# Kernel optimization log

Measured on AMD Instinct MI355X. Metric: run time of the kernel, lower is better.

The kernel has to match this reference:

```python
import jax, jax.numpy as jnp
import numpy as np

BLOCKSIZE = 4096
OUT_FEATURES = 16384
IN_FEATURES = 4096
BATCH, SEQ = 4, 2048


def setup_inputs() -> dict:
    key = jax.random.key(0)
    k_x, k_w, k_a, k_b = jax.random.split(key, 4)
    x = jax.random.normal(k_x, (BATCH, SEQ, IN_FEATURES), dtype=jnp.float32)
    # quantized int8 weight stored as indices into the 256-entry codebook
    weight_q = jax.random.randint(k_w, (OUT_FEATURES, IN_FEATURES), 0, 256, dtype=jnp.int32)
    n_blocks = (OUT_FEATURES * IN_FEATURES) // BLOCKSIZE  # 16384
    absmax = jax.random.uniform(k_a, (n_blocks,), dtype=jnp.float32) + 0.5
    # bitsandbytes dynamic-map code: a sorted table of values in [-1, 1]
    code = jnp.linspace(-1.0, 1.0, 256, dtype=jnp.float32)
    bias = jax.random.normal(k_b, (OUT_FEATURES,), dtype=jnp.float32) * 0.02
    return {"x": x, "weight_q": weight_q, "absmax": absmax, "code": code, "bias": bias}


def dequantize_blockwise(weight_q, absmax, code):
    # codebook lookup then per-block absmax scaling
    flat = code[weight_q.reshape(-1)]                      # [out*in]
    flat = flat.reshape(-1, BLOCKSIZE) * absmax[:, None]   # [n_blocks, blocksize]
    return flat.reshape(weight_q.shape)                    # [out, in]


def reference(x, weight_q, absmax, code, bias):
    w = dequantize_blockwise(weight_q, absmax, code)       # [out, in] fp32
    # F.linear(x, w, bias) = x @ w.T + bias
    return jnp.einsum("bsi,oi->bso", x, w) + bias
```

## Files before the change

kernel.cpp:

```cpp
#include <hip/hip_runtime.h>
#include <hip/hip_bf16.h>
#include <stdint.h>

#define M_TOTAL 8192
#define N_TOTAL 16384
#define K_TOTAL 4096

#define BM 256
#define BN 256
#define BK 64
#define NKT (K_TOTAL / BK)

using f32x4  = __attribute__((ext_vector_type(4))) float;
using bf16x8 = __attribute__((ext_vector_type(8))) short;

#define UNROLL _Pragma("unroll")

__device__ __forceinline__ unsigned short f2bf(float f) {
    union { float f; unsigned u; } v; v.f = f;
    unsigned r = v.u + 0x7fffu + ((v.u >> 16) & 1u);
    return (unsigned short)(r >> 16);
}

__device__ __forceinline__ void gload_lds16(const void* g, void* l) {
    __builtin_amdgcn_global_load_lds(
        (const __attribute__((address_space(1))) unsigned int*)g,
        (__attribute__((address_space(3))) unsigned int*)l,
        16, 0, 0);
}

__global__ void dequant_w_kernel(const int* __restrict__ q,
                                 const float* __restrict__ am,
                                 const float* __restrict__ code,
                                 unsigned short* __restrict__ wb) {
    __shared__ float lc[256];
    if (threadIdx.x < 256) lc[threadIdx.x] = code[threadIdx.x];
    __syncthreads();
    const int total = (N_TOTAL / 4) * K_TOTAL;
    const int stride = gridDim.x * blockDim.x;
    for (int i = blockIdx.x * blockDim.x + threadIdx.x; i < total; i += stride) {
        int4 v = reinterpret_cast<const int4*>(q)[i];
        float a = am[i >> 10];
        ushort4 o;
        o.x = f2bf(lc[v.x & 255] * a);
        o.y = f2bf(lc[v.y & 255] * a);
        o.z = f2bf(lc[v.z & 255] * a);
        o.w = f2bf(lc[v.w & 255] * a);
        reinterpret_cast<ushort4*>(wb)[i] = o;
    }
}

__global__ void cvt_x_kernel(const float* __restrict__ x,
                             unsigned short* __restrict__ xb) {
    const int total = (M_TOTAL * K_TOTAL) / 4;
    const int stride = gridDim.x * blockDim.x;
    for (int i = blockIdx.x * blockDim.x + threadIdx.x; i < total; i += stride) {
        float4 v = reinterpret_cast<const float4*>(x)[i];
        ushort4 o;
        o.x = f2bf(v.x); o.y = f2bf(v.y); o.z = f2bf(v.z); o.w = f2bf(v.w);
        reinterpret_cast<ushort4*>(xb)[i] = o;
    }
}

#define LOAD_A(DST, BUFI, MH)                                                     \
    UNROLL for (int mf = 0; mf < 4; ++mf)                                         \
        UNROLL for (int ks = 0; ks < 2; ++ks)                                     \
            DST[mf][ks] = *reinterpret_cast<const bf16x8*>(                       \
                &sA[BUFI][((MH)*128 + arow_base + mf*16)*BK +                     \
                          (((ks*4 + rslot_hi) ^ rslot_xor)*8)]);

#define LOAD_B(DST, BUFI, NH)                                                     \
    UNROLL for (int nf = 0; nf < 2; ++nf)                                         \
        UNROLL for (int ks = 0; ks < 2; ++ks)                                     \
            DST[nf][ks] = *reinterpret_cast<const bf16x8*>(                       \
                &sB[BUFI][((NH)*128 + brow_base + nf*16)*BK +                     \
                          (((ks*4 + rslot_hi) ^ rslot_xor)*8)]);

#define MFMA_Q(MH, NH, AR, BR)                                                    \
    UNROLL for (int mf = 0; mf < 4; ++mf)                                         \
        UNROLL for (int nf = 0; nf < 2; ++nf) {                                   \
            acc[MH][mf][NH][nf] = __builtin_amdgcn_mfma_f32_16x16x32_bf16(        \
                AR[mf][0], BR[nf][0], acc[MH][mf][NH][nf], 0, 0, 0);              \
            acc[MH][mf][NH][nf] = __builtin_amdgcn_mfma_f32_16x16x32_bf16(        \
                AR[mf][1], BR[nf][1], acc[MH][mf][NH][nf], 0, 0, 0);              \
        }

#define PH_BAR()                                                                  \
    asm volatile("s_waitcnt lgkmcnt(0)" ::: "memory");                            \
    __builtin_amdgcn_s_barrier();                                                 \
    asm volatile("" ::: "memory");

#define TILE_CORE(BUF, STG, TS, LDNEXT)                                           \
                                                 \
    LOAD_B(b1_r, BUF, 1);                                                         \
    __builtin_amdgcn_s_setprio(1); MFMA_Q(0, 0, a0_r, b0_r);                      \
    __builtin_amdgcn_s_setprio(0);                                                \
    PH_BAR();                                                                     \
                              \
    LOAD_A(a1_r, BUF, 1);                                                         \
    if (STG) { stA(0,0,TS,BUF); stA(0,1,TS,BUF);                                  \
               stB(0,0,TS,BUF); stB(0,1,TS,BUF); }                                \
    __builtin_amdgcn_s_setprio(1); MFMA_Q(0, 1, a0_r, b1_r);                      \
    __builtin_amdgcn_s_setprio(0);                                                \
    PH_BAR();                                                                     \
                  \
    if (LDNEXT) { LOAD_A(a0_r, BUF^1, 0); }                                       \
    if (STG) { stB(1,0,TS,BUF); stB(1,1,TS,BUF); }                                \
    __builtin_amdgcn_s_setprio(1); MFMA_Q(1, 1, a1_r, b1_r);                      \
    __builtin_amdgcn_s_setprio(0);                                                \
    PH_BAR();                                                                     \
             \
    if (STG) { stA(1,0,TS,BUF); stA(1,1,TS,BUF); }                                \
    __builtin_amdgcn_s_setprio(1); MFMA_Q(1, 0, a1_r, b0_r);                      \
    __builtin_amdgcn_s_setprio(0);                                                \
    if (LDNEXT) { LOAD_B(b0_r, BUF^1, 0); }

#define GATE(VMN)                                                                 \
    asm volatile("s_waitcnt lgkmcnt(0) vmcnt(" #VMN ")" ::: "memory");            \
    __builtin_amdgcn_s_barrier();                                                 \
    asm volatile("" ::: "memory");

__global__ __launch_bounds__(512, 2) void gemm_pp_kernel(
        const unsigned short* __restrict__ A,
        const unsigned short* __restrict__ B,
        const float* __restrict__ bias,
        float* __restrict__ C) {
    __shared__ __align__(16) unsigned short sA[2][BM * BK];
    __shared__ __align__(16) unsigned short sB[2][BN * BK];

    const int nwg = gridDim.x;
    const int bid = blockIdx.x;
    const int wg  = (bid & 7) * (nwg >> 3) + (bid >> 3);
    const int nbn = N_TOTAL / BN;
    const int brow = (wg / nbn) * BM;
    const int bcol = (wg % nbn) * BN;

    const int tid  = threadIdx.x;
    const int wid  = tid >> 6;
    const int lane = tid & 63;
    const int wm   = wid >> 2;
    const int wn   = wid & 3;

    const int srow = wid * 8 + (lane >> 3);
    const int scol = ((lane & 7) ^ (lane >> 3)) * 8;
    const unsigned short* Asrc = A + (long long)(brow + srow) * K_TOTAL + scol;
    const unsigned short* Bsrc = B + (long long)(bcol + srow) * K_TOTAL + scol;

    auto stA = [&](int h, int j, int kt, int b) {
        gload_lds16(Asrc + (long long)(h*128 + j*64) * K_TOTAL + kt*BK,
                    &sA[b][(h*128 + j*64)*BK + wid*512]);
    };
    auto stB = [&](int h, int j, int kt, int b) {
        gload_lds16(Bsrc + (long long)(h*128 + j*64) * K_TOTAL + kt*BK,
                    &sB[b][(h*128 + j*64)*BK + wid*512]);
    };

    const int arow_base = wm * 64 + (lane & 15);
    const int brow_base = wn * 32 + (lane & 15);
    const int rslot_hi  = lane >> 4;
    const int rslot_xor = lane & 7;

    f32x4 acc[2][4][2][2];
    UNROLL for (int mh = 0; mh < 2; ++mh)
        UNROLL for (int mf = 0; mf < 4; ++mf)
            UNROLL for (int nh = 0; nh < 2; ++nh)
                UNROLL for (int nf = 0; nf < 2; ++nf)
                    acc[mh][mf][nh][nf] = (f32x4){0.f, 0.f, 0.f, 0.f};

    bf16x8 a0_r[4][2], a1_r[4][2];
    bf16x8 b0_r[2][2], b1_r[2][2];

    stA(0,0,0,0); stA(0,1,0,0); stA(1,0,0,0); stA(1,1,0,0);
    stB(0,0,0,0); stB(0,1,0,0); stB(1,0,0,0); stB(1,1,0,0);
    stA(0,0,1,1); stA(0,1,1,1); stA(1,0,1,1); stA(1,1,1,1);
    stB(0,0,1,1); stB(0,1,1,1); stB(1,0,1,1); stB(1,1,1,1);
    asm volatile("s_waitcnt vmcnt(8)" ::: "memory");
    __builtin_amdgcn_s_barrier();
    asm volatile("" ::: "memory");
    LOAD_A(a0_r, 0, 0);
    LOAD_B(b0_r, 0, 0);

    for (int it = 0; it < NKT/2 - 1; ++it) {
        const int t0 = 2*it;
        TILE_CORE(0, 1, t0 + 2, 1)
        GATE(8)
        TILE_CORE(1, 1, t0 + 3, 1)
        GATE(8)
    }
    TILE_CORE(0, 0, 0, 1)
    GATE(0)
    TILE_CORE(1, 0, 0, 0)

    const int crow0 = (lane >> 4) * 4;
    const int ccol  = lane & 15;
    UNROLL for (int mh = 0; mh < 2; ++mh)
        UNROLL for (int mf = 0; mf < 4; ++mf) {
            const long long row0 = (long long)brow + mh*128 + wm*64 + mf*16 + crow0;
            UNROLL for (int nh = 0; nh < 2; ++nh)
                UNROLL for (int nf = 0; nf < 2; ++nf) {
                    const int col = bcol + nh*128 + wn*32 + nf*16 + ccol;
                    const float bv = bias[col];
                    UNROLL for (int r = 0; r < 4; ++r)
                        C[(row0 + r) * N_TOTAL + col] = acc[mh][mf][nh][nf][r] + bv;
                }
        }
}

extern "C" void kernel_launch(void* const* d_in, const int* in_sizes, int n_in,
                              void* d_out, int out_size, void* d_ws, size_t ws_size,
                              hipStream_t stream) {
    const float* x      = (const float*)d_in[0];
    const int*   wq     = (const int*)  d_in[1];
    const float* absmax = (const float*)d_in[2];
    const float* code   = (const float*)d_in[3];
    const float* bias   = (const float*)d_in[4];
    float* out = (float*)d_out;

    unsigned short* wb = (unsigned short*)d_ws;
    unsigned short* xb = wb + (size_t)N_TOTAL * K_TOTAL;

    dequant_w_kernel<<<2048, 256, 0, stream>>>(wq, absmax, code, wb);
    cvt_x_kernel   <<<2048, 256, 0, stream>>>(x, xb);

    dim3 grid((M_TOTAL / BM) * (N_TOTAL / BN));
    gemm_pp_kernel<<<grid, 512, 0, stream>>>(xb, wb, bias, out);
}
```

Baseline: 1.117 ms.

## Restructure GEMM main loop into two-phase schedule with single A register set

Replaces the four-phase per-tile schedule (three barriers, double A register sets, next-tile fragment prefetch) with a two-phase schedule: each half loads its A half and both B fragments, then issues two MFMA quadrants. The A second-half global-to-LDS stage for the next tile is issued one phase early into the other buffer, and vmcnt gates are adjusted to match. This drops one A register array and two barriers per tile to cut VGPR pressure and sync overhead, at the cost of less overlap between LDS reads and MFMAs within a tile.

```diff
diff --git a/kernel.cpp b/kernel.cpp
--- a/kernel.cpp
+++ b/kernel.cpp
@@ -90,37 +90,29 @@
     __builtin_amdgcn_s_barrier();                                                 \
     asm volatile("" ::: "memory");
 
-#define TILE_CORE(BUF, STG, TS, LDNEXT)                                           \
-                                                 \
-    LOAD_B(b1_r, BUF, 1);                                                         \
-    __builtin_amdgcn_s_setprio(1); MFMA_Q(0, 0, a0_r, b0_r);                      \
+#define TILE2(BUF, AH1T, TS)                                                      \
+    LOAD_A(a_r, BUF, 0); LOAD_B(b0_r, BUF, 0); LOAD_B(b1_r, BUF, 1);              \
+    if ((AH1T) >= 0) { stA(1,0,AH1T,(BUF)^1); stA(1,1,AH1T,(BUF)^1); }            \
+    __builtin_amdgcn_s_setprio(1);                                                \
+    MFMA_Q(0, 0, a_r, b0_r);                                                      \
+    MFMA_Q(0, 1, a_r, b1_r);                                                      \
     __builtin_amdgcn_s_setprio(0);                                                \
     PH_BAR();                                                                     \
-                              \
-    LOAD_A(a1_r, BUF, 1);                                                         \
-    if (STG) { stA(0,0,TS,BUF); stA(0,1,TS,BUF);                                  \
-               stB(0,0,TS,BUF); stB(0,1,TS,BUF); }                                \
-    __builtin_amdgcn_s_setprio(1); MFMA_Q(0, 1, a0_r, b1_r);                      \
-    __builtin_amdgcn_s_setprio(0);                                                \
-    PH_BAR();                                                                     \
-                  \
-    if (LDNEXT) { LOAD_A(a0_r, BUF^1, 0); }                                       \
-    if (STG) { stB(1,0,TS,BUF); stB(1,1,TS,BUF); }                                \
-    __builtin_amdgcn_s_setprio(1); MFMA_Q(1, 1, a1_r, b1_r);                      \
-    __builtin_amdgcn_s_setprio(0);                                                \
-    PH_BAR();                                                                     \
-             \
-    if (STG) { stA(1,0,TS,BUF); stA(1,1,TS,BUF); }                                \
-    __builtin_amdgcn_s_setprio(1); MFMA_Q(1, 0, a1_r, b0_r);                      \
-    __builtin_amdgcn_s_setprio(0);                                                \
-    if (LDNEXT) { LOAD_B(b0_r, BUF^1, 0); }
+    LOAD_A(a_r, BUF, 1);                                                          \
+    if ((TS) >= 0) { stA(0,0,TS,BUF); stA(0,1,TS,BUF);                            \
+                     stB(0,0,TS,BUF); stB(0,1,TS,BUF);                            \
+                     stB(1,0,TS,BUF); stB(1,1,TS,BUF); }                          \
+    __builtin_amdgcn_s_setprio(1);                                                \
+    MFMA_Q(1, 1, a_r, b1_r);                                                      \
+    MFMA_Q(1, 0, a_r, b0_r);                                                      \
+    __builtin_amdgcn_s_setprio(0);
 
 #define GATE(VMN)                                                                 \
     asm volatile("s_waitcnt lgkmcnt(0) vmcnt(" #VMN ")" ::: "memory");            \
     __builtin_amdgcn_s_barrier();                                                 \
     asm volatile("" ::: "memory");
 
-__global__ __launch_bounds__(512, 2) void gemm_pp_kernel(
+__global__ __launch_bounds__(512, 2) void gemm_p2_kernel(
         const unsigned short* __restrict__ A,
         const unsigned short* __restrict__ B,
         const float* __restrict__ bias,
@@ -167,29 +159,27 @@
                 UNROLL for (int nf = 0; nf < 2; ++nf)
                     acc[mh][mf][nh][nf] = (f32x4){0.f, 0.f, 0.f, 0.f};
 
-    bf16x8 a0_r[4][2], a1_r[4][2];
+    bf16x8 a_r[4][2];
     bf16x8 b0_r[2][2], b1_r[2][2];
 
     stA(0,0,0,0); stA(0,1,0,0); stA(1,0,0,0); stA(1,1,0,0);
     stB(0,0,0,0); stB(0,1,0,0); stB(1,0,0,0); stB(1,1,0,0);
-    stA(0,0,1,1); stA(0,1,1,1); stA(1,0,1,1); stA(1,1,1,1);
+    stA(0,0,1,1); stA(0,1,1,1);
     stB(0,0,1,1); stB(0,1,1,1); stB(1,0,1,1); stB(1,1,1,1);
-    asm volatile("s_waitcnt vmcnt(8)" ::: "memory");
+    asm volatile("s_waitcnt vmcnt(6)" ::: "memory");
     __builtin_amdgcn_s_barrier();
     asm volatile("" ::: "memory");
-    LOAD_A(a0_r, 0, 0);
-    LOAD_B(b0_r, 0, 0);
 
     for (int it = 0; it < NKT/2 - 1; ++it) {
         const int t0 = 2*it;
-        TILE_CORE(0, 1, t0 + 2, 1)
-        GATE(8)
-        TILE_CORE(1, 1, t0 + 3, 1)
-        GATE(8)
+        TILE2(0, t0 + 1, t0 + 2)
+        GATE(6)
+        TILE2(1, t0 + 2, t0 + 3)
+        GATE(6)
     }
-    TILE_CORE(0, 0, 0, 1)
+    TILE2(0, 63, -1)
     GATE(0)
-    TILE_CORE(1, 0, 0, 0)
+    TILE2(1, -1, -1)
 
     const int crow0 = (lane >> 4) * 4;
     const int ccol  = lane & 15;
@@ -223,5 +213,5 @@
     cvt_x_kernel   <<<2048, 256, 0, stream>>>(x, xb);
 
     dim3 grid((M_TOTAL / BM) * (N_TOTAL / BN));
-    gemm_pp_kernel<<<grid, 512, 0, stream>>>(xb, wb, bias, out);
-}
+    gemm_p2_kernel<<<grid, 512, 0, stream>>>(xb, wb, bias, out);
+}
```

Result: no change. 1.113 ms (-0.3%).
